# Kernel tuning notes

Hardware: AMD Instinct MI355X
Metric: run time of the kernel (lower is better)

## Reference

```python
import jax, jax.numpy as jnp
import numpy as np
import math

B, C = 16, 32
LOOKBACK, PRED = 1024, 256
DELAY, STRIDE = 64, 1
DPD = 128            # dist_projection_dim
THETA = 1.0
TOTAL = LOOKBACK + PRED                      # 1280
U = TOTAL // STRIDE - DELAY + 1              # 1217 unfolded windows
UL = int(LOOKBACK / TOTAL * U)               # 973
UP = U - UL                                  # 244 unfolded_pred_len
MAXLEN = max(1100, TOTAL)                    # 1280 (learnable PE length)


def _sinusoid_pe():
    pos = np.arange(MAXLEN, dtype=np.float32)[:, None]
    div = np.exp(np.arange(0, DPD, 2, dtype=np.float32) * (-math.log(10000.0) / DPD))
    pe = np.zeros((MAXLEN, DPD), np.float32)
    pe[:, 0::2] = np.sin(pos * div)
    pe[:, 1::2] = np.cos(pos * div)
    return jnp.asarray(pe)


def setup_inputs() -> dict:
    key = jax.random.key(0)
    ks = jax.random.split(key, 8)
    n = lambda i, sh, sc=1.0: jax.random.normal(ks[i], sh, dtype=jnp.float32) * sc
    return dict(
        lookback_series=n(0, (B, C, LOOKBACK)),
        focal_point_series=n(1, (B, C, PRED)),
        W_proj=n(2, (DELAY, DPD), 0.05),
        b_proj=jnp.zeros((DPD,), jnp.float32),
        pe=_sinusoid_pe(),                       # learnable PE, sinusoid-initialized
        ln_g=jnp.ones((DPD,), jnp.float32),
        ln_b=jnp.zeros((DPD,), jnp.float32),
        W1=n(3, (DELAY * UP, PRED), 0.01),       # undelay linear 1: 15616 -> 256
        b1=jnp.zeros((PRED,), jnp.float32),
        W2=n(4, (PRED, PRED), 0.05),             # undelay linear 2: 256 -> 256
        b2=jnp.zeros((PRED,), jnp.float32),
    )


def _layernorm(x, g, b):
    m = jnp.mean(x, axis=-1, keepdims=True)
    v = jnp.var(x, axis=-1, keepdims=True)
    return (x - m) * jax.lax.rsqrt(v + 1e-5) * g + b


def reference(lookback_series, focal_point_series, W_proj, b_proj, pe, ln_g, ln_b, W1, b1, W2, b2):
    # concat + time-delay unfold -> [B, C, U, DELAY]
    series = jnp.concatenate([lookback_series, focal_point_series], axis=-1)
    idx = jnp.arange(U)[:, None] * STRIDE + jnp.arange(DELAY)[None, :]
    win = series[:, :, idx]

    focal = win[:, :, U - (UP + 1):, :]          # [B,C,UP+1,DELAY]
    hist = win[:, :, :U - (UP + 1), :]           # [B,C,972,DELAY]
    td_hist = hist[:, :, :-1, :]                 # K/V history windows [B,C,971,DELAY]
    td_next = hist[:, :, 1:, :]                  # one-step-shifted values

    k = td_hist @ W_proj + b_proj                # [B,C,T,DPD]
    q = focal[:, :, :-1, :] @ W_proj + b_proj    # [B,C,UP,DPD]
    T = k.shape[2]
    k = k + pe[:T]
    q = q + pe[T:T + UP]
    k = _layernorm(k, ln_g, ln_b)
    q = _layernorm(q, ln_g, ln_b)

    scale = THETA / math.sqrt(DPD)
    attn = jax.nn.softmax(jnp.einsum('bcqe,bcke->bcqk', q, k) * scale, axis=-1)
    preds = jnp.einsum('bcqk,bckd->bcqd', attn, td_next)   # [B,C,UP,DELAY]

    flat = preds.reshape(B, C, UP * DELAY)
    h = jax.nn.gelu(flat @ W1 + b1, approximate=False)     # torch nn.GELU (exact)
    return h @ W2 + b2                                      # [B,C,PRED]
```

## Files before the change

### kernel.cpp

```cpp
#include <hip/hip_runtime.h>
#include <hip/hip_bf16.h>

#define LOOK   1024
#define PREDN  256
#define TOT    1280
#define SBLEN  1296
#define DPD    128
#define NK     971
#define RPB    122
#define NKT    16
#define SCALE  0.08838834764831845f

typedef __attribute__((ext_vector_type(8))) short short8;
typedef __attribute__((ext_vector_type(4))) float f32x4;

__device__ __forceinline__ unsigned short f2bu(float x) {
    union { __hip_bfloat16 b; unsigned short u; } v;
    v.b = __float2bfloat16(x);
    return v.u;
}
__device__ __forceinline__ unsigned int pack2(float a, float b) {
    return (unsigned int)f2bu(a) | ((unsigned int)f2bu(b) << 16);
}

__device__ __forceinline__ short8 load_sfrag(const unsigned short* s0, int idx0) {
    const unsigned int* p = (const unsigned int*)s0 + (idx0 >> 1);
    const unsigned int sh = (idx0 & 1) << 4;
    unsigned int w0 = p[0], w1 = p[1], w2 = p[2], w3 = p[3], w4 = p[4];
    union { unsigned int u[4]; short8 s; } v;
    v.u[0] = (unsigned int)((((unsigned long long)w1 << 32) | w0) >> sh);
    v.u[1] = (unsigned int)((((unsigned long long)w2 << 32) | w1) >> sh);
    v.u[2] = (unsigned int)((((unsigned long long)w3 << 32) | w2) >> sh);
    v.u[3] = (unsigned int)((((unsigned long long)w4 << 32) | w3) >> sh);
    return v.s;
}
__device__ __forceinline__ short8 ld_b64x2(const unsigned short* p) {
    union { unsigned long long q[2]; short8 s; } v;
    v.q[0] = *(const unsigned long long*)p;
    v.q[1] = *(const unsigned long long*)(p + 4);
    return v.s;
}

__device__ __forceinline__ void proj_tile(
    const unsigned short* s_sb0, const unsigned short* s_wpb,
    const unsigned int* s_gb, unsigned short* s_kb,
    const float* __restrict__ peb,
    int widx, int perow, int rowkb, int quad, int kcol)
{
    short8 bw0 = load_sfrag(s_sb0, widx + 8 * quad);
    short8 bw1 = load_sfrag(s_sb0, widx + 32 + 8 * quad);
    f32x4 pc[8];
    #pragma unroll
    for (int mt = 0; mt < 8; ++mt) pc[mt] = (f32x4){0.f, 0.f, 0.f, 0.f};
    const int k7 = kcol & 7;
    #pragma unroll
    for (int mt = 0; mt < 8; ++mt) {
        int e = 16 * mt + kcol;
        short8 a0 = *(const short8*)&s_wpb[e * 64 + ((quad ^ k7) << 3)];
        short8 a1 = *(const short8*)&s_wpb[e * 64 + (((4 + quad) ^ k7) << 3)];
        pc[mt] = __builtin_amdgcn_mfma_f32_16x16x32_bf16(a0, bw0, pc[mt], 0, 0, 0);
        pc[mt] = __builtin_amdgcn_mfma_f32_16x16x32_bf16(a1, bw1, pc[mt], 0, 0, 0);
    }
    float x[8][4];
    float sm = 0.f, sq = 0.f;
    #pragma unroll
    for (int mt = 0; mt < 8; ++mt) {
        float4 pv = *(const float4*)&peb[perow * 128 + 16 * mt + 4 * quad];
        x[mt][0] = pc[mt][0] + pv.x; x[mt][1] = pc[mt][1] + pv.y;
        x[mt][2] = pc[mt][2] + pv.z; x[mt][3] = pc[mt][3] + pv.w;
        #pragma unroll
        for (int r = 0; r < 4; ++r) { sm += x[mt][r]; sq += x[mt][r] * x[mt][r]; }
    }
    sm += __shfl_xor(sm, 16); sq += __shfl_xor(sq, 16);
    sm += __shfl_xor(sm, 32); sq += __shfl_xor(sq, 32);
    float mean = sm * (1.0f / 128.0f);
    float var  = sq * (1.0f / 128.0f) - mean * mean;
    float rs   = rsqrtf(var + 1e-5f);
    #pragma unroll
    for (int mt = 0; mt < 8; ++mt) {
        uint4 gb = *(const uint4*)&s_gb[16 * mt + 4 * quad];
        unsigned int gw[4] = {gb.x, gb.y, gb.z, gb.w};
        float y[4];
        #pragma unroll
        for (int r = 0; r < 4; ++r) {
            float g = __uint_as_float(gw[r] << 16);
            float b = __uint_as_float(gw[r] & 0xFFFF0000u);
            y[r] = (x[mt][r] - mean) * rs * g + b;
        }
        unsigned long long w = ((unsigned long long)pack2(y[2], y[3]) << 32) | pack2(y[0], y[1]);
        *(unsigned long long*)&s_kb[rowkb * 132 + 16 * mt + 4 * quad] = w;
    }
}

__global__ __launch_bounds__(256, 3)
void attn_kernel(const float* __restrict__ lookback,
                 const float* __restrict__ focal,
                 const float* __restrict__ Wp,
                 const float* __restrict__ peb,
                 const float* __restrict__ lng,
                 const float* __restrict__ lnb,
                 unsigned short* __restrict__ flat_hi,
                 unsigned short* __restrict__ flat_lo)
{
    __shared__ unsigned short s_sb0[SBLEN];
    __shared__ unsigned short s_wpb[128 * 64];
    __shared__ unsigned short s_kb[64 * 132];
    __shared__ unsigned short s_P[128 * 68];
    __shared__ unsigned int   s_gb[DPD];

    const int t    = threadIdx.x;
    const int pair = blockIdx.x >> 1;
    const int hb   = blockIdx.x & 1;
    const int lane = t & 63;
    const int wave = t >> 6;
    const int quad = lane >> 4;
    const int kcol = lane & 15;

    {
        if (t < 256) {
            float4 v = ((const float4*)(lookback + pair * LOOK))[t];
            s_sb0[4 * t]     = f2bu(v.x);
            s_sb0[4 * t + 1] = f2bu(v.y);
            s_sb0[4 * t + 2] = f2bu(v.z);
            s_sb0[4 * t + 3] = f2bu(v.w);
        }
        if (t < 64) {
            float4 v = ((const float4*)(focal + pair * PREDN))[t];
            s_sb0[LOOK + 4 * t]     = f2bu(v.x);
            s_sb0[LOOK + 4 * t + 1] = f2bu(v.y);
            s_sb0[LOOK + 4 * t + 2] = f2bu(v.z);
            s_sb0[LOOK + 4 * t + 3] = f2bu(v.w);
        }
        if (t < SBLEN - TOT) s_sb0[TOT + t] = 0;
        #pragma unroll
        for (int j = 0; j < 32; ++j) {
            int fl = j * 256 + t;
            int k = fl >> 7, e = fl & 127;
            s_wpb[e * 64 + (((k >> 3) ^ (e & 7)) << 3) + (k & 7)] = f2bu(Wp[fl]);
        }
        if (t < DPD)
            s_gb[t] = (unsigned int)f2bu(lng[t]) | ((unsigned int)f2bu(lnb[t]) << 16);
    }
    __syncthreads();

    short8 aq[2][4];
    for (int qt = 0; qt < 2; ++qt) {
        proj_tile(s_sb0, s_wpb, s_gb, s_kb, peb,
                  972 + hb * RPB + 64 * qt + 16 * wave + kcol,
                  971 + hb * RPB + 64 * qt + 16 * wave + kcol,
                  16 * wave + kcol, quad, kcol);
        __syncthreads();
        if ((wave >> 1) == qt) {
            #pragma unroll
            for (int ntQ = 0; ntQ < 2; ++ntQ) {
                int g = 2 * wave + ntQ - 4 * qt;
                #pragma unroll
                for (int kc = 0; kc < 4; ++kc)
                    aq[ntQ][kc] = ld_b64x2(&s_kb[(16 * g + kcol) * 132 + 32 * kc + 8 * quad]);
            }
        }
        __syncthreads();
    }

    float mrow[2] = {-3.0e38f, -3.0e38f};
    float lrow[2] = {0.0f, 0.0f};
    f32x4 o[2][4];
    #pragma unroll
    for (int a = 0; a < 2; ++a)
        #pragma unroll
        for (int b = 0; b < 4; ++b) o[a][b] = (f32x4){0.f, 0.f, 0.f, 0.f};

    for (int tile = 0; tile < NKT; ++tile) {
        const int j0 = tile * 64;

        proj_tile(s_sb0, s_wpb, s_gb, s_kb, peb,
                  j0 + 16 * wave + kcol, j0 + 16 * wave + kcol,
                  16 * wave + kcol, quad, kcol);
        __syncthreads();

        f32x4 sacc[2][4];
        #pragma unroll
        for (int a = 0; a < 2; ++a)
            #pragma unroll
            for (int b = 0; b < 4; ++b) sacc[a][b] = (f32x4){0.f, 0.f, 0.f, 0.f};
        #pragma unroll
        for (int kc = 0; kc < 4; ++kc) {
            short8 ak[4];
            #pragma unroll
            for (int mtK = 0; mtK < 4; ++mtK)
                ak[mtK] = ld_b64x2(&s_kb[(16 * mtK + kcol) * 132 + 32 * kc + 8 * quad]);
            #pragma unroll
            for (int ntQ = 0; ntQ < 2; ++ntQ)
                #pragma unroll
                for (int mtK = 0; mtK < 4; ++mtK)
                    sacc[ntQ][mtK] = __builtin_amdgcn_mfma_f32_16x16x32_bf16(
                        ak[mtK], aq[ntQ][kc], sacc[ntQ][mtK], 0, 0, 0);
        }

        float alf[2];
        #pragma unroll
        for (int ntQ = 0; ntQ < 2; ++ntQ) {
            float P[4][4];
            float mx = -1.0e30f;
            #pragma unroll
            for (int mtK = 0; mtK < 4; ++mtK)
                #pragma unroll
                for (int r = 0; r < 4; ++r) {
                    int key = j0 + 16 * mtK + 4 * quad + r;
                    float s = (key < NK) ? sacc[ntQ][mtK][r] * SCALE : -1.0e30f;
                    P[mtK][r] = s;
                    mx = fmaxf(mx, s);
                }
            mx = fmaxf(mx, __shfl_xor(mx, 16));
            mx = fmaxf(mx, __shfl_xor(mx, 32));
            float mo = mrow[ntQ];
            float mn = fmaxf(mo, mx);
            float a  = __expf(mo - mn);
            float ss = 0.f;
            #pragma unroll
            for (int mtK = 0; mtK < 4; ++mtK)
                #pragma unroll
                for (int r = 0; r < 4; ++r) {
                    P[mtK][r] = __expf(P[mtK][r] - mn);
                    ss += P[mtK][r];
                }
            ss += __shfl_xor(ss, 16);
            ss += __shfl_xor(ss, 32);
            lrow[ntQ] = lrow[ntQ] * a + ss;
            mrow[ntQ] = mn;
            alf[ntQ]  = a;
            const int pbase = (16 * (2 * wave + ntQ) + kcol) * 68;
            #pragma unroll
            for (int mtK = 0; mtK < 4; ++mtK) {
                unsigned long long w = ((unsigned long long)pack2(P[mtK][2], P[mtK][3]) << 32)
                                       | pack2(P[mtK][0], P[mtK][1]);
                *(unsigned long long*)&s_P[pbase + 16 * mtK + 4 * quad] = w;
            }
        }

        #pragma unroll
        for (int ntQ = 0; ntQ < 2; ++ntQ)
            #pragma unroll
            for (int r = 0; r < 4; ++r) {
                float af = __shfl(alf[ntQ], 20 * quad + r);
                #pragma unroll
                for (int ntD = 0; ntD < 4; ++ntD) o[ntQ][ntD][r] *= af;
            }

        short8 xf[4][2];
        #pragma unroll
        for (int ntD = 0; ntD < 4; ++ntD)
            #pragma unroll
            for (int kc2 = 0; kc2 < 2; ++kc2)
                xf[ntD][kc2] = load_sfrag(s_sb0, j0 + 1 + 32 * kc2 + 8 * quad + 16 * ntD + kcol);
        #pragma unroll
        for (int ntQ = 0; ntQ < 2; ++ntQ) {
            const int pbase = (16 * (2 * wave + ntQ) + kcol) * 68;
            short8 ap[2];
            #pragma unroll
            for (int kc2 = 0; kc2 < 2; ++kc2)
                ap[kc2] = ld_b64x2(&s_P[pbase + 32 * kc2 + 8 * quad]);
            #pragma unroll
            for (int ntD = 0; ntD < 4; ++ntD)
                #pragma unroll
                for (int kc2 = 0; kc2 < 2; ++kc2)
                    o[ntQ][ntD] = __builtin_amdgcn_mfma_f32_16x16x32_bf16(
                        ap[kc2], xf[ntD][kc2], o[ntQ][ntD], 0, 0, 0);
        }
        __syncthreads();
    }

    float inv[2] = {1.0f / lrow[0], 1.0f / lrow[1]};
    #pragma unroll
    for (int ntQ = 0; ntQ < 2; ++ntQ)
        #pragma unroll
        for (int r = 0; r < 4; ++r) {
            float li = __shfl(inv[ntQ], 20 * quad + r);
            int brow = 32 * wave + 16 * ntQ + 4 * quad + r;
            if (brow < RPB) {
                int base = pair * 15616 + (hb * RPB + brow) * 64 + kcol;
                #pragma unroll
                for (int ntD = 0; ntD < 4; ++ntD) {
                    float v = o[ntQ][ntD][r] * li;
                    unsigned short h = f2bu(v);
                    float vh = __uint_as_float((unsigned int)h << 16);
                    flat_hi[base + 16 * ntD] = h;
                    flat_lo[base + 16 * ntD] = f2bu(v - vh);
                }
            }
        }
}

__global__ void peb_kernel(const float* __restrict__ pe,
                           const float* __restrict__ bp,
                           float* __restrict__ peb)
{
    int i = blockIdx.x * 256 + threadIdx.x;
    peb[i] = pe[i] + bp[i & 127];
}

__global__ __launch_bounds__(256, 2)
void mlp1_kernel(const unsigned short* __restrict__ Ah,
                 const unsigned short* __restrict__ Al,
                 const float* __restrict__ W1,
                 float* __restrict__ part)
{
    const int bid = blockIdx.x;
    const int bm = bid & 7, bn = (bid >> 3) & 3, bz = bid >> 5;
    const int m0 = bm * 64, n0 = bn * 64;
    const int t0 = bz * 30 + (bz < 8 ? bz : 8);
    const int nt = (bz < 8) ? 31 : 30;

    __shared__ unsigned short sAh[64 * 40];
    __shared__ unsigned short sAl[64 * 40];
    __shared__ unsigned short sBh[64 * 44];
    __shared__ unsigned short sBl[64 * 44];

    const int t = threadIdx.x;
    const int wv = t >> 6, lane = t & 63;
    const int quad = lane >> 4, kcol = lane & 15;
    const int ar = t >> 2, ac8 = (t & 3) * 8;
    const int bk = t >> 3, bn8 = (t & 7) * 8;

    f32x4 acc[4];
    #pragma unroll
    for (int i = 0; i < 4; ++i) acc[i] = (f32x4){0.f, 0.f, 0.f, 0.f};

    for (int tt = 0; tt < nt; ++tt) {
        const int kc = (t0 + tt) * 32;
        *(uint4*)&sAh[ar * 40 + ac8] = *(const uint4*)(Ah + (m0 + ar) * 15616 + kc + ac8);
        *(uint4*)&sAl[ar * 40 + ac8] = *(const uint4*)(Al + (m0 + ar) * 15616 + kc + ac8);
        {
            const float* wp = W1 + (kc + bk) * 256 + n0 + bn8;
            float4 wa = *(const float4*)wp;
            float4 wb = *(const float4*)(wp + 4);
            float vv[8] = {wa.x, wa.y, wa.z, wa.w, wb.x, wb.y, wb.z, wb.w};
            #pragma unroll
            for (int i = 0; i < 8; ++i) {
                unsigned short h = f2bu(vv[i]);
                float vh = __uint_as_float((unsigned int)h << 16);
                sBh[(bn8 + i) * 44 + bk] = h;
                sBl[(bn8 + i) * 44 + bk] = f2bu(vv[i] - vh);
            }
        }
        __syncthreads();
        short8 bh = ld_b64x2(&sBh[(16 * wv + kcol) * 44 + quad * 8]);
        short8 bl = ld_b64x2(&sBl[(16 * wv + kcol) * 44 + quad * 8]);
        #pragma unroll
        for (int mt = 0; mt < 4; ++mt) {
            short8 ah = *(const short8*)&sAh[(16 * mt + kcol) * 40 + quad * 8];
            short8 al = *(const short8*)&sAl[(16 * mt + kcol) * 40 + quad * 8];
            acc[mt] = __builtin_amdgcn_mfma_f32_16x16x32_bf16(ah, bh, acc[mt], 0, 0, 0);
            acc[mt] = __builtin_amdgcn_mfma_f32_16x16x32_bf16(al, bh, acc[mt], 0, 0, 0);
            acc[mt] = __builtin_amdgcn_mfma_f32_16x16x32_bf16(ah, bl, acc[mt], 0, 0, 0);
        }
        __syncthreads();
    }
    float* dst = part + bz * (512 * 256);
    #pragma unroll
    for (int mt = 0; mt < 4; ++mt)
        #pragma unroll
        for (int r = 0; r < 4; ++r)
            dst[(m0 + 16 * mt + 4 * quad + r) * 256 + n0 + 16 * wv + kcol] = acc[mt][r];
}

__global__ void gelu_kernel(const float* __restrict__ part,
                            const float* __restrict__ b1,
                            float* __restrict__ H)
{
    const int i = blockIdx.x * 256 + threadIdx.x;
    float s = 0.0f;
    #pragma unroll
    for (int ks = 0; ks < 16; ++ks) s += part[ks * 131072 + i];
    s += b1[i & 255];
    H[i] = 0.5f * s * (1.0f + erff(s * 0.7071067811865475f));
}

__global__ __launch_bounds__(256, 2)
void mlp2_kernel(const float* __restrict__ H,
                 const float* __restrict__ W2,
                 const float* __restrict__ b2,
                 float* __restrict__ out)
{
    const int bm = blockIdx.x & 7, bn = blockIdx.x >> 3;
    const int m0 = bm * 64, n0 = bn * 64;
    __shared__ float sA[64 * 36];
    __shared__ float sB[32 * 68];
    float acc[16];
    #pragma unroll
    for (int i = 0; i < 16; ++i) acc[i] = 0.0f;

    const int wv = threadIdx.x >> 6, ln = threadIdx.x & 63;
    const int tm = 4 * wv + (ln >> 4), tn = ln & 15;
    const int r = threadIdx.x >> 3;
    const int c4 = (threadIdx.x & 7) * 4;
    const int c8 = (threadIdx.x & 7) * 8;

    for (int tt = 0; tt < 8; ++tt) {
        const int kc = tt * 32;
        *(float4*)&sA[r * 36 + c4]        = *(const float4*)(H + (m0 + r) * 256 + kc + c4);
        *(float4*)&sA[(r + 32) * 36 + c4] = *(const float4*)(H + (m0 + r + 32) * 256 + kc + c4);
        *(float4*)&sB[r * 68 + c8]     = *(const float4*)(W2 + (kc + r) * 256 + n0 + c8);
        *(float4*)&sB[r * 68 + c8 + 4] = *(const float4*)(W2 + (kc + r) * 256 + n0 + c8 + 4);
        __syncthreads();
        #pragma unroll
        for (int kg = 0; kg < 8; ++kg) {
            float4 a[4], b[4];
            #pragma unroll
            for (int i = 0; i < 4; ++i) a[i] = *(const float4*)&sA[(4 * tm + i) * 36 + 4 * kg];
            #pragma unroll
            for (int j = 0; j < 4; ++j) b[j] = *(const float4*)&sB[(4 * kg + j) * 68 + 4 * tn];
            #pragma unroll
            for (int i = 0; i < 4; ++i) {
                acc[4*i+0] += a[i].x*b[0].x + a[i].y*b[1].x + a[i].z*b[2].x + a[i].w*b[3].x;
                acc[4*i+1] += a[i].x*b[0].y + a[i].y*b[1].y + a[i].z*b[2].y + a[i].w*b[3].y;
                acc[4*i+2] += a[i].x*b[0].z + a[i].y*b[1].z + a[i].z*b[2].z + a[i].w*b[3].z;
                acc[4*i+3] += a[i].x*b[0].w + a[i].y*b[1].w + a[i].z*b[2].w + a[i].w*b[3].w;
            }
        }
        __syncthreads();
    }
    #pragma unroll
    for (int i = 0; i < 4; ++i)
        #pragma unroll
        for (int j = 0; j < 4; ++j) {
            const int m = m0 + 4 * tm + i, n = n0 + 4 * tn + j;
            out[m * 256 + n] = acc[4 * i + j] + b2[n];
        }
}

extern "C" void kernel_launch(void* const* d_in, const int* in_sizes, int n_in,
                              void* d_out, int out_size, void* d_ws, size_t ws_size,
                              hipStream_t stream) {
    (void)in_sizes; (void)n_in; (void)out_size; (void)ws_size;
    const float* lookback = (const float*)d_in[0];
    const float* focal    = (const float*)d_in[1];
    const float* Wp       = (const float*)d_in[2];
    const float* bp       = (const float*)d_in[3];
    const float* pe       = (const float*)d_in[4];
    const float* lng      = (const float*)d_in[5];
    const float* lnb      = (const float*)d_in[6];
    const float* W1       = (const float*)d_in[7];
    const float* b1       = (const float*)d_in[8];
    const float* W2       = (const float*)d_in[9];
    const float* b2       = (const float*)d_in[10];

    unsigned short* flat_hi = (unsigned short*)d_ws;
    unsigned short* flat_lo = flat_hi + 512 * 15616;
    float* part = (float*)(flat_lo + 512 * 15616);
    float* H    = part + 16 * 512 * 256;
    float* peb  = part;

    hipLaunchKernelGGL(peb_kernel, dim3(640), dim3(256), 0, stream, pe, bp, peb);
    hipLaunchKernelGGL(attn_kernel, dim3(1024), dim3(256), 0, stream,
                       lookback, focal, Wp, peb, lng, lnb, flat_hi, flat_lo);
    hipLaunchKernelGGL(mlp1_kernel, dim3(512), dim3(256), 0, stream,
                       flat_hi, flat_lo, W1, part);
    hipLaunchKernelGGL(gelu_kernel, dim3(512), dim3(256), 0, stream, part, b1, H);
    hipLaunchKernelGGL(mlp2_kernel, dim3(32), dim3(256), 0, stream, H, W2, b2,
                       (float*)d_out);
}
```

Baseline: 323.2 us.

## Process all queries per series in one attention block; widen MLP1 M tile

The attention kernel now runs one block per (batch, channel) series covering all 244 query rows, instead of two blocks each covering 122. This removes the duplicated K projection and LayerNorm work, which the two half-blocks previously each recomputed for all 971 keys. The cost is halving the grid to 512 blocks, dropping to 2 blocks per CU, and raising register and LDS use for the larger Q, score and output fragments. MLP1 also moves to 128-row M tiles with 256 blocks, so each converted W1 tile is reused across twice as many rows, at the cost of less parallelism.

```diff
diff --git a/kernel.cpp b/kernel.cpp
--- a/kernel.cpp
+++ b/kernel.cpp
@@ -7,7 +7,7 @@
 #define SBLEN  1296
 #define DPD    128
 #define NK     971
-#define RPB    122
+#define RPBT   244
 #define NKT    16
 #define SCALE  0.08838834764831845f
 
@@ -92,7 +92,7 @@
     }
 }
 
-__global__ __launch_bounds__(256, 3)
+__global__ __launch_bounds__(256, 2)
 void attn_kernel(const float* __restrict__ lookback,
                  const float* __restrict__ focal,
                  const float* __restrict__ Wp,
@@ -105,12 +105,11 @@
     __shared__ unsigned short s_sb0[SBLEN];
     __shared__ unsigned short s_wpb[128 * 64];
     __shared__ unsigned short s_kb[64 * 132];
-    __shared__ unsigned short s_P[128 * 68];
+    __shared__ unsigned short s_P[256 * 68];
     __shared__ unsigned int   s_gb[DPD];
 
     const int t    = threadIdx.x;
-    const int pair = blockIdx.x >> 1;
-    const int hb   = blockIdx.x & 1;
+    const int pair = blockIdx.x;
     const int lane = t & 63;
     const int wave = t >> 6;
     const int quad = lane >> 4;
@@ -143,30 +142,28 @@
     }
     __syncthreads();
 
-    short8 aq[2][4];
-    for (int qt = 0; qt < 2; ++qt) {
+    short8 aq[4][4];
+    for (int qt = 0; qt < 4; ++qt) {
         proj_tile(s_sb0, s_wpb, s_gb, s_kb, peb,
-                  972 + hb * RPB + 64 * qt + 16 * wave + kcol,
-                  971 + hb * RPB + 64 * qt + 16 * wave + kcol,
+                  972 + 64 * qt + 16 * wave + kcol,
+                  971 + 64 * qt + 16 * wave + kcol,
                   16 * wave + kcol, quad, kcol);
         __syncthreads();
-        if ((wave >> 1) == qt) {
-            #pragma unroll
-            for (int ntQ = 0; ntQ < 2; ++ntQ) {
-                int g = 2 * wave + ntQ - 4 * qt;
+        if (wave == qt) {
+            #pragma unroll
+            for (int ntQ = 0; ntQ < 4; ++ntQ)
                 #pragma unroll
                 for (int kc = 0; kc < 4; ++kc)
-                    aq[ntQ][kc] = ld_b64x2(&s_kb[(16 * g + kcol) * 132 + 32 * kc + 8 * quad]);
-            }
-        }
-        __syncthreads();
-    }
-
-    float mrow[2] = {-3.0e38f, -3.0e38f};
-    float lrow[2] = {0.0f, 0.0f};
-    f32x4 o[2][4];
-    #pragma unroll
-    for (int a = 0; a < 2; ++a)
+                    aq[ntQ][kc] = ld_b64x2(&s_kb[(16 * ntQ + kcol) * 132 + 32 * kc + 8 * quad]);
+        }
+        __syncthreads();
+    }
+
+    float mrow[4] = {-3.0e38f, -3.0e38f, -3.0e38f, -3.0e38f};
+    float lrow[4] = {0.0f, 0.0f, 0.0f, 0.0f};
+    f32x4 o[4][4];
+    #pragma unroll
+    for (int a = 0; a < 4; ++a)
         #pragma unroll
         for (int b = 0; b < 4; ++b) o[a][b] = (f32x4){0.f, 0.f, 0.f, 0.f};
 
@@ -178,9 +175,9 @@
                   16 * wave + kcol, quad, kcol);
         __syncthreads();
 
-        f32x4 sacc[2][4];
-        #pragma unroll
-        for (int a = 0; a < 2; ++a)
+        f32x4 sacc[4][4];
+        #pragma unroll
+        for (int a = 0; a < 4; ++a)
             #pragma unroll
             for (int b = 0; b < 4; ++b) sacc[a][b] = (f32x4){0.f, 0.f, 0.f, 0.f};
         #pragma unroll
@@ -190,16 +187,16 @@
             for (int mtK = 0; mtK < 4; ++mtK)
                 ak[mtK] = ld_b64x2(&s_kb[(16 * mtK + kcol) * 132 + 32 * kc + 8 * quad]);
             #pragma unroll
-            for (int ntQ = 0; ntQ < 2; ++ntQ)
+            for (int ntQ = 0; ntQ < 4; ++ntQ)
                 #pragma unroll
                 for (int mtK = 0; mtK < 4; ++mtK)
                     sacc[ntQ][mtK] = __builtin_amdgcn_mfma_f32_16x16x32_bf16(
                         ak[mtK], aq[ntQ][kc], sacc[ntQ][mtK], 0, 0, 0);
         }
 
-        float alf[2];
-        #pragma unroll
-        for (int ntQ = 0; ntQ < 2; ++ntQ) {
+        float alf[4];
+        #pragma unroll
+        for (int ntQ = 0; ntQ < 4; ++ntQ) {
             float P[4][4];
             float mx = -1.0e30f;
             #pragma unroll
@@ -229,7 +226,7 @@
             lrow[ntQ] = lrow[ntQ] * a + ss;
             mrow[ntQ] = mn;
             alf[ntQ]  = a;
-            const int pbase = (16 * (2 * wave + ntQ) + kcol) * 68;
+            const int pbase = (16 * (4 * wave + ntQ) + kcol) * 68;
             #pragma unroll
             for (int mtK = 0; mtK < 4; ++mtK) {
                 unsigned long long w = ((unsigned long long)pack2(P[mtK][2], P[mtK][3]) << 32)
@@ -239,7 +236,7 @@
         }
 
         #pragma unroll
-        for (int ntQ = 0; ntQ < 2; ++ntQ)
+        for (int ntQ = 0; ntQ < 4; ++ntQ)
             #pragma unroll
             for (int r = 0; r < 4; ++r) {
                 float af = __shfl(alf[ntQ], 20 * quad + r);
@@ -254,8 +251,8 @@
             for (int kc2 = 0; kc2 < 2; ++kc2)
                 xf[ntD][kc2] = load_sfrag(s_sb0, j0 + 1 + 32 * kc2 + 8 * quad + 16 * ntD + kcol);
         #pragma unroll
-        for (int ntQ = 0; ntQ < 2; ++ntQ) {
-            const int pbase = (16 * (2 * wave + ntQ) + kcol) * 68;
+        for (int ntQ = 0; ntQ < 4; ++ntQ) {
+            const int pbase = (16 * (4 * wave + ntQ) + kcol) * 68;
             short8 ap[2];
             #pragma unroll
             for (int kc2 = 0; kc2 < 2; ++kc2)
@@ -270,15 +267,15 @@
         __syncthreads();
     }
 
-    float inv[2] = {1.0f / lrow[0], 1.0f / lrow[1]};
-    #pragma unroll
-    for (int ntQ = 0; ntQ < 2; ++ntQ)
+    float inv[4] = {1.0f / lrow[0], 1.0f / lrow[1], 1.0f / lrow[2], 1.0f / lrow[3]};
+    #pragma unroll
+    for (int ntQ = 0; ntQ < 4; ++ntQ)
         #pragma unroll
         for (int r = 0; r < 4; ++r) {
             float li = __shfl(inv[ntQ], 20 * quad + r);
-            int brow = 32 * wave + 16 * ntQ + 4 * quad + r;
-            if (brow < RPB) {
-                int base = pair * 15616 + (hb * RPB + brow) * 64 + kcol;
+            int brow = 64 * wave + 16 * ntQ + 4 * quad + r;
+            if (brow < RPBT) {
+                int base = pair * 15616 + brow * 64 + kcol;
                 #pragma unroll
                 for (int ntD = 0; ntD < 4; ++ntD) {
                     float v = o[ntQ][ntD][r] * li;
@@ -306,30 +303,32 @@
                  float* __restrict__ part)
 {
     const int bid = blockIdx.x;
-    const int bm = bid & 7, bn = (bid >> 3) & 3, bz = bid >> 5;
-    const int m0 = bm * 64, n0 = bn * 64;
+    const int bm = bid & 3, bn = (bid >> 2) & 3, bz = bid >> 4;
+    const int m0 = bm * 128, n0 = bn * 64;
     const int t0 = bz * 30 + (bz < 8 ? bz : 8);
     const int nt = (bz < 8) ? 31 : 30;
 
-    __shared__ unsigned short sAh[64 * 40];
-    __shared__ unsigned short sAl[64 * 40];
+    __shared__ unsigned short sAh[128 * 40];
+    __shared__ unsigned short sAl[128 * 40];
     __shared__ unsigned short sBh[64 * 44];
     __shared__ unsigned short sBl[64 * 44];
 
     const int t = threadIdx.x;
     const int wv = t >> 6, lane = t & 63;
     const int quad = lane >> 4, kcol = lane & 15;
-    const int ar = t >> 2, ac8 = (t & 3) * 8;
+    const int ar = t >> 1, ac16 = (t & 1) * 16;
     const int bk = t >> 3, bn8 = (t & 7) * 8;
 
-    f32x4 acc[4];
-    #pragma unroll
-    for (int i = 0; i < 4; ++i) acc[i] = (f32x4){0.f, 0.f, 0.f, 0.f};
+    f32x4 acc[8];
+    #pragma unroll
+    for (int i = 0; i < 8; ++i) acc[i] = (f32x4){0.f, 0.f, 0.f, 0.f};
 
     for (int tt = 0; tt < nt; ++tt) {
         const int kc = (t0 + tt) * 32;
-        *(uint4*)&sAh[ar * 40 + ac8] = *(const uint4*)(Ah + (m0 + ar) * 15616 + kc + ac8);
-        *(uint4*)&sAl[ar * 40 + ac8] = *(const uint4*)(Al + (m0 + ar) * 15616 + kc + ac8);
+        *(uint4*)&sAh[ar * 40 + ac16]     = *(const uint4*)(Ah + (m0 + ar) * 15616 + kc + ac16);
+        *(uint4*)&sAh[ar * 40 + ac16 + 8] = *(const uint4*)(Ah + (m0 + ar) * 15616 + kc + ac16 + 8);
+        *(uint4*)&sAl[ar * 40 + ac16]     = *(const uint4*)(Al + (m0 + ar) * 15616 + kc + ac16);
+        *(uint4*)&sAl[ar * 40 + ac16 + 8] = *(const uint4*)(Al + (m0 + ar) * 15616 + kc + ac16 + 8);
         {
             const float* wp = W1 + (kc + bk) * 256 + n0 + bn8;
             float4 wa = *(const float4*)wp;
@@ -347,7 +346,7 @@
         short8 bh = ld_b64x2(&sBh[(16 * wv + kcol) * 44 + quad * 8]);
         short8 bl = ld_b64x2(&sBl[(16 * wv + kcol) * 44 + quad * 8]);
         #pragma unroll
-        for (int mt = 0; mt < 4; ++mt) {
+        for (int mt = 0; mt < 8; ++mt) {
             short8 ah = *(const short8*)&sAh[(16 * mt + kcol) * 40 + quad * 8];
             short8 al = *(const short8*)&sAl[(16 * mt + kcol) * 40 + quad * 8];
             acc[mt] = __builtin_amdgcn_mfma_f32_16x16x32_bf16(ah, bh, acc[mt], 0, 0, 0);
@@ -358,7 +357,7 @@
     }
     float* dst = part + bz * (512 * 256);
     #pragma unroll
-    for (int mt = 0; mt < 4; ++mt)
+    for (int mt = 0; mt < 8; ++mt)
         #pragma unroll
         for (int r = 0; r < 4; ++r)
             dst[(m0 + 16 * mt + 4 * quad + r) * 256 + n0 + 16 * wv + kcol] = acc[mt][r];
@@ -452,9 +451,9 @@
     float* peb  = part;
 
     hipLaunchKernelGGL(peb_kernel, dim3(640), dim3(256), 0, stream, pe, bp, peb);
-    hipLaunchKernelGGL(attn_kernel, dim3(1024), dim3(256), 0, stream,
+    hipLaunchKernelGGL(attn_kernel, dim3(512), dim3(256), 0, stream,
                        lookback, focal, Wp, peb, lng, lnb, flat_hi, flat_lo);
-    hipLaunchKernelGGL(mlp1_kernel, dim3(512), dim3(256), 0, stream,
+    hipLaunchKernelGGL(mlp1_kernel, dim3(256), dim3(256), 0, stream,
                        flat_hi, flat_lo, W1, part);
     hipLaunchKernelGGL(gelu_kernel, dim3(512), dim3(256), 0, stream, part, b1, H);
     hipLaunchKernelGGL(mlp2_kernel, dim3(32), dim3(256), 0, stream, H, W2, b2,
```

New measurement: 281.5 us. -12.9%, faster.

## Drop online-softmax max tracking, use per-wave P slots, widen mlp1 M tile

Applied to the files above, without the earlier changes.

The attention kernel stops tracking a running max and rescaling the output accumulators. Because q and k are layer-normalised, scores are bounded, so it exponentiates clamped scores directly and only accumulates the row sum. This removes cross-lane max reductions and the per-tile rescale shuffles. The P staging buffer shrinks to one 16-row slot per wave that is reused across both query sub-tiles, lowering LDS use. Separately, the mlp1 GEMM now uses 128-row M tiles with half as many blocks, giving more reuse of each converted W1 tile. The risks are lower occupancy for mlp1 and reliance on the score bound with a clamp at 80.

```diff
diff --git a/kernel.cpp b/kernel.cpp
--- a/kernel.cpp
+++ b/kernel.cpp
@@ -105,7 +105,7 @@
     __shared__ unsigned short s_sb0[SBLEN];
     __shared__ unsigned short s_wpb[128 * 64];
     __shared__ unsigned short s_kb[64 * 132];
-    __shared__ unsigned short s_P[128 * 68];
+    __shared__ unsigned short s_Pw[4 * 16 * 68];
     __shared__ unsigned int   s_gb[DPD];
 
     const int t    = threadIdx.x;
@@ -153,7 +153,7 @@
         if ((wave >> 1) == qt) {
             #pragma unroll
             for (int ntQ = 0; ntQ < 2; ++ntQ) {
-                int g = 2 * wave + ntQ - 4 * qt;
+                int g = 2 * (wave & 1) + ntQ;
                 #pragma unroll
                 for (int kc = 0; kc < 4; ++kc)
                     aq[ntQ][kc] = ld_b64x2(&s_kb[(16 * g + kcol) * 132 + 32 * kc + 8 * quad]);
@@ -162,13 +162,14 @@
         __syncthreads();
     }
 
-    float mrow[2] = {-3.0e38f, -3.0e38f};
     float lrow[2] = {0.0f, 0.0f};
     f32x4 o[2][4];
     #pragma unroll
     for (int a = 0; a < 2; ++a)
         #pragma unroll
         for (int b = 0; b < 4; ++b) o[a][b] = (f32x4){0.f, 0.f, 0.f, 0.f};
+
+    unsigned short* slot = &s_Pw[wave * (16 * 68)];
 
     for (int tile = 0; tile < NKT; ++tile) {
         const int j0 = tile * 64;
@@ -197,69 +198,39 @@
                         ak[mtK], aq[ntQ][kc], sacc[ntQ][mtK], 0, 0, 0);
         }
 
-        float alf[2];
+        short8 xf[4][2];
+        #pragma unroll
+        for (int ntD = 0; ntD < 4; ++ntD)
+            #pragma unroll
+            for (int kc2 = 0; kc2 < 2; ++kc2)
+                xf[ntD][kc2] = load_sfrag(s_sb0, j0 + 1 + 32 * kc2 + 8 * quad + 16 * ntD + kcol);
+
         #pragma unroll
         for (int ntQ = 0; ntQ < 2; ++ntQ) {
-            float P[4][4];
-            float mx = -1.0e30f;
-            #pragma unroll
-            for (int mtK = 0; mtK < 4; ++mtK)
+            float ss = 0.f;
+            unsigned long long pk[4];
+            #pragma unroll
+            for (int mtK = 0; mtK < 4; ++mtK) {
+                float P[4];
                 #pragma unroll
                 for (int r = 0; r < 4; ++r) {
                     int key = j0 + 16 * mtK + 4 * quad + r;
-                    float s = (key < NK) ? sacc[ntQ][mtK][r] * SCALE : -1.0e30f;
-                    P[mtK][r] = s;
-                    mx = fmaxf(mx, s);
+                    float s = (key < NK) ? fminf(sacc[ntQ][mtK][r] * SCALE, 80.0f) : -80.0f;
+                    P[r] = __expf(s);
+                    ss += P[r];
                 }
-            mx = fmaxf(mx, __shfl_xor(mx, 16));
-            mx = fmaxf(mx, __shfl_xor(mx, 32));
-            float mo = mrow[ntQ];
-            float mn = fmaxf(mo, mx);
-            float a  = __expf(mo - mn);
-            float ss = 0.f;
-            #pragma unroll
-            for (int mtK = 0; mtK < 4; ++mtK)
-                #pragma unroll
-                for (int r = 0; r < 4; ++r) {
-                    P[mtK][r] = __expf(P[mtK][r] - mn);
-                    ss += P[mtK][r];
-                }
+                pk[mtK] = ((unsigned long long)pack2(P[2], P[3]) << 32) | pack2(P[0], P[1]);
+            }
             ss += __shfl_xor(ss, 16);
             ss += __shfl_xor(ss, 32);
-            lrow[ntQ] = lrow[ntQ] * a + ss;
-            mrow[ntQ] = mn;
-            alf[ntQ]  = a;
-            const int pbase = (16 * (2 * wave + ntQ) + kcol) * 68;
-            #pragma unroll
-            for (int mtK = 0; mtK < 4; ++mtK) {
-                unsigned long long w = ((unsigned long long)pack2(P[mtK][2], P[mtK][3]) << 32)
-                                       | pack2(P[mtK][0], P[mtK][1]);
-                *(unsigned long long*)&s_P[pbase + 16 * mtK + 4 * quad] = w;
-            }
-        }
-
-        #pragma unroll
-        for (int ntQ = 0; ntQ < 2; ++ntQ)
-            #pragma unroll
-            for (int r = 0; r < 4; ++r) {
-                float af = __shfl(alf[ntQ], 20 * quad + r);
-                #pragma unroll
-                for (int ntD = 0; ntD < 4; ++ntD) o[ntQ][ntD][r] *= af;
-            }
-
-        short8 xf[4][2];
-        #pragma unroll
-        for (int ntD = 0; ntD < 4; ++ntD)
+            lrow[ntQ] += ss;
+            #pragma unroll
+            for (int mtK = 0; mtK < 4; ++mtK)
+                *(unsigned long long*)&slot[kcol * 68 + 16 * mtK + 4 * quad] = pk[mtK];
+            short8 ap[2];
             #pragma unroll
             for (int kc2 = 0; kc2 < 2; ++kc2)
-                xf[ntD][kc2] = load_sfrag(s_sb0, j0 + 1 + 32 * kc2 + 8 * quad + 16 * ntD + kcol);
-        #pragma unroll
-        for (int ntQ = 0; ntQ < 2; ++ntQ) {
-            const int pbase = (16 * (2 * wave + ntQ) + kcol) * 68;
-            short8 ap[2];
-            #pragma unroll
-            for (int kc2 = 0; kc2 < 2; ++kc2)
-                ap[kc2] = ld_b64x2(&s_P[pbase + 32 * kc2 + 8 * quad]);
+                ap[kc2] = ld_b64x2(&slot[kcol * 68 + 32 * kc2 + 8 * quad]);
             #pragma unroll
             for (int ntD = 0; ntD < 4; ++ntD)
                 #pragma unroll
@@ -306,30 +277,32 @@
                  float* __restrict__ part)
 {
     const int bid = blockIdx.x;
-    const int bm = bid & 7, bn = (bid >> 3) & 3, bz = bid >> 5;
-    const int m0 = bm * 64, n0 = bn * 64;
+    const int bm = bid & 3, bn = (bid >> 2) & 3, bz = bid >> 4;
+    const int m0 = bm * 128, n0 = bn * 64;
     const int t0 = bz * 30 + (bz < 8 ? bz : 8);
     const int nt = (bz < 8) ? 31 : 30;
 
-    __shared__ unsigned short sAh[64 * 40];
-    __shared__ unsigned short sAl[64 * 40];
+    __shared__ unsigned short sAh[128 * 40];
+    __shared__ unsigned short sAl[128 * 40];
     __shared__ unsigned short sBh[64 * 44];
     __shared__ unsigned short sBl[64 * 44];
 
     const int t = threadIdx.x;
     const int wv = t >> 6, lane = t & 63;
     const int quad = lane >> 4, kcol = lane & 15;
-    const int ar = t >> 2, ac8 = (t & 3) * 8;
+    const int ar = t >> 1, ac16 = (t & 1) * 16;
     const int bk = t >> 3, bn8 = (t & 7) * 8;
 
-    f32x4 acc[4];
-    #pragma unroll
-    for (int i = 0; i < 4; ++i) acc[i] = (f32x4){0.f, 0.f, 0.f, 0.f};
+    f32x4 acc[8];
+    #pragma unroll
+    for (int i = 0; i < 8; ++i) acc[i] = (f32x4){0.f, 0.f, 0.f, 0.f};
 
     for (int tt = 0; tt < nt; ++tt) {
         const int kc = (t0 + tt) * 32;
-        *(uint4*)&sAh[ar * 40 + ac8] = *(const uint4*)(Ah + (m0 + ar) * 15616 + kc + ac8);
-        *(uint4*)&sAl[ar * 40 + ac8] = *(const uint4*)(Al + (m0 + ar) * 15616 + kc + ac8);
+        *(uint4*)&sAh[ar * 40 + ac16]     = *(const uint4*)(Ah + (m0 + ar) * 15616 + kc + ac16);
+        *(uint4*)&sAh[ar * 40 + ac16 + 8] = *(const uint4*)(Ah + (m0 + ar) * 15616 + kc + ac16 + 8);
+        *(uint4*)&sAl[ar * 40 + ac16]     = *(const uint4*)(Al + (m0 + ar) * 15616 + kc + ac16);
+        *(uint4*)&sAl[ar * 40 + ac16 + 8] = *(const uint4*)(Al + (m0 + ar) * 15616 + kc + ac16 + 8);
         {
             const float* wp = W1 + (kc + bk) * 256 + n0 + bn8;
             float4 wa = *(const float4*)wp;
@@ -347,7 +320,7 @@
         short8 bh = ld_b64x2(&sBh[(16 * wv + kcol) * 44 + quad * 8]);
         short8 bl = ld_b64x2(&sBl[(16 * wv + kcol) * 44 + quad * 8]);
         #pragma unroll
-        for (int mt = 0; mt < 4; ++mt) {
+        for (int mt = 0; mt < 8; ++mt) {
             short8 ah = *(const short8*)&sAh[(16 * mt + kcol) * 40 + quad * 8];
             short8 al = *(const short8*)&sAl[(16 * mt + kcol) * 40 + quad * 8];
             acc[mt] = __builtin_amdgcn_mfma_f32_16x16x32_bf16(ah, bh, acc[mt], 0, 0, 0);
@@ -358,7 +331,7 @@
     }
     float* dst = part + bz * (512 * 256);
     #pragma unroll
-    for (int mt = 0; mt < 4; ++mt)
+    for (int mt = 0; mt < 8; ++mt)
         #pragma unroll
         for (int r = 0; r < 4; ++r)
             dst[(m0 + 16 * mt + 4 * quad + r) * 256 + n0 + 16 * wv + kcol] = acc[mt][r];
@@ -454,7 +427,7 @@
     hipLaunchKernelGGL(peb_kernel, dim3(640), dim3(256), 0, stream, pe, bp, peb);
     hipLaunchKernelGGL(attn_kernel, dim3(1024), dim3(256), 0, stream,
                        lookback, focal, Wp, peb, lng, lnb, flat_hi, flat_lo);
-    hipLaunchKernelGGL(mlp1_kernel, dim3(512), dim3(256), 0, stream,
+    hipLaunchKernelGGL(mlp1_kernel, dim3(256), dim3(256), 0, stream,
                        flat_hi, flat_lo, W1, part);
     hipLaunchKernelGGL(gelu_kernel, dim3(512), dim3(256), 0, stream, part, b1, H);
     hipLaunchKernelGGL(mlp2_kernel, dim3(32), dim3(256), 0, stream, H, W2, b2,
```

After: 324.9 us. Within noise of the previous version (+0.5%).
